# Kernel optimization log

Measured on AMD Instinct MI355X. Metric: run time of the kernel, lower is better.

The kernel has to match this reference:

```python
import jax, jax.numpy as jnp
import numpy as np

D_MODEL = 1024
NUM_HEADS = 16
D_K = D_MODEL // NUM_HEADS
D_FF = 4096
EPS = 1e-6


def setup_inputs() -> dict:
    key = jax.random.key(0)
    ks = jax.random.split(key, 12)
    B, S = 4, 1024
    s = 1.0 / np.sqrt(D_MODEL)
    return {
        "x": jax.random.normal(ks[0], (B, S, D_MODEL), dtype=jnp.float32),
        "ln1_g": jnp.ones((D_MODEL,), jnp.float32),
        "ln1_b": jnp.zeros((D_MODEL,), jnp.float32),
        "wq": jax.random.normal(ks[1], (D_MODEL, D_MODEL), jnp.float32) * s,
        "wk": jax.random.normal(ks[2], (D_MODEL, D_MODEL), jnp.float32) * s,
        "wv": jax.random.normal(ks[3], (D_MODEL, D_MODEL), jnp.float32) * s,
        "wo": jax.random.normal(ks[4], (D_MODEL, D_MODEL), jnp.float32) * s,
        "ln2_g": jnp.ones((D_MODEL,), jnp.float32),
        "ln2_b": jnp.zeros((D_MODEL,), jnp.float32),
        "w1": jax.random.normal(ks[5], (D_MODEL, D_FF), jnp.float32) * s,
        "b1": jnp.zeros((D_FF,), jnp.float32),
        "w2": jax.random.normal(ks[6], (D_FF, D_MODEL), jnp.float32) * (1.0 / np.sqrt(D_FF)),
        "b2": jnp.zeros((D_MODEL,), jnp.float32),
    }


def _layernorm(x, g, b):
    mu = jnp.mean(x, axis=-1, keepdims=True)
    var = jnp.var(x, axis=-1, keepdims=True)
    return (x - mu) * jax.lax.rsqrt(var + EPS) * g + b


def _mha(x, wq, wk, wv, wo):
    B, S, _ = x.shape
    # project and split heads: [B,S,D] -> [B,H,S,Dk]
    q = (x @ wq).reshape(B, S, NUM_HEADS, D_K).transpose(0, 2, 1, 3)
    k = (x @ wk).reshape(B, S, NUM_HEADS, D_K).transpose(0, 2, 1, 3)
    v = (x @ wv).reshape(B, S, NUM_HEADS, D_K).transpose(0, 2, 1, 3)
    scores = jnp.einsum("bhqd,bhkd->bhqk", q, k) / np.sqrt(D_K).astype(np.float32)
    attn = jax.nn.softmax(scores, axis=-1)  # no mask: source forwards mask=None
    out = jnp.einsum("bhqk,bhkd->bhqd", attn, v)
    out = out.transpose(0, 2, 1, 3).reshape(B, S, D_MODEL)
    return out @ wo


def reference(x, ln1_g, ln1_b, wq, wk, wv, wo, ln2_g, ln2_b, w1, b1, w2, b2):
    x1 = _layernorm(x, ln1_g, ln1_b)
    x = x + _mha(x1, wq, wk, wv, wo)  # dropout identity (eval)
    x2 = _layernorm(x, ln2_g, ln2_b)
    ffn = jax.nn.relu(x2 @ w1 + b1) @ w2 + b2
    return x + ffn
```

## Files before the change

### kernel.cpp

```cpp
#include <hip/hip_runtime.h>

typedef __bf16 bf16;
typedef __bf16 bf16x8 __attribute__((ext_vector_type(8)));
typedef __bf16 bf16x4 __attribute__((ext_vector_type(4)));
typedef float f32x4 __attribute__((ext_vector_type(4)));

__device__ __forceinline__ void gload_lds16(const void* g, void* l) {
  __builtin_amdgcn_global_load_lds(
      (const __attribute__((address_space(1))) unsigned int*)g,
      (__attribute__((address_space(3))) unsigned int*)l, 16, 0, 0);
}

__global__ __launch_bounds__(256) void prep_kernel(
    const float* __restrict__ wq, const float* __restrict__ wk,
    const float* __restrict__ wv, const float* __restrict__ wo,
    const float* __restrict__ w1, const float* __restrict__ w2,
    bf16* __restrict__ wTqkv, bf16* __restrict__ wTo,
    bf16* __restrict__ wT1, bf16* __restrict__ wT2,
    const float* __restrict__ x, const float* __restrict__ g,
    const float* __restrict__ b, bf16* __restrict__ y) {
  const int id = blockIdx.x;
  if (id < 1024) {
    const int w = threadIdx.x >> 6, lane = threadIdx.x & 63;
    const int row = id * 4 + w;
    const float* xr = x + (size_t)row * 1024;
    float4 v[4];
    float s = 0.f, sq = 0.f;
#pragma unroll
    for (int c = 0; c < 4; c++) {
      v[c] = *reinterpret_cast<const float4*>(xr + c * 256 + lane * 4);
      s += v[c].x + v[c].y + v[c].z + v[c].w;
      sq += v[c].x * v[c].x + v[c].y * v[c].y + v[c].z * v[c].z + v[c].w * v[c].w;
    }
#pragma unroll
    for (int d = 32; d >= 1; d >>= 1) {
      s += __shfl_xor(s, d, 64);
      sq += __shfl_xor(sq, d, 64);
    }
    const float mu = s * (1.f / 1024.f);
    const float rs = rsqrtf(sq * (1.f / 1024.f) - mu * mu + 1e-6f);
#pragma unroll
    for (int c = 0; c < 4; c++) {
      float4 gv = *reinterpret_cast<const float4*>(g + c * 256 + lane * 4);
      float4 bv = *reinterpret_cast<const float4*>(b + c * 256 + lane * 4);
      bf16x4 ov;
      ov[0] = (bf16)((v[c].x - mu) * rs * gv.x + bv.x);
      ov[1] = (bf16)((v[c].y - mu) * rs * gv.y + bv.y);
      ov[2] = (bf16)((v[c].z - mu) * rs * gv.z + bv.z);
      ov[3] = (bf16)((v[c].w - mu) * rs * gv.w + bv.w);
      *reinterpret_cast<bf16x4*>(y + (size_t)row * 1024 + c * 256 + lane * 4) = ov;
    }
    return;
  }
  __shared__ float tile[32][33];
  const int idx = id - 1024;
  const float* src;
  bf16* dst;
  int R, C, bx, by;
  if (idx < 4096) {
    const int m = idx >> 10, r = idx & 1023;
    src = m == 0 ? wq : m == 1 ? wk : m == 2 ? wv : wo;
    dst = m == 3 ? wTo : wTqkv + (size_t)m * 1024 * 1024;
    R = 1024; C = 1024; bx = r & 31; by = r >> 5;
  } else if (idx < 8192) {
    const int r = idx - 4096;
    src = w1; dst = wT1; R = 1024; C = 4096;
    bx = r & 127; by = r >> 7;
  } else {
    const int r = idx - 8192;
    src = w2; dst = wT2; R = 4096; C = 1024;
    bx = r & 31; by = r >> 5;
  }
  const int tx = threadIdx.x & 31, ty = threadIdx.x >> 5;
  const int c0 = bx * 32, r0 = by * 32;
#pragma unroll
  for (int i = 0; i < 4; i++)
    tile[ty + i * 8][tx] = src[(size_t)(r0 + ty + i * 8) * C + c0 + tx];
  __syncthreads();
#pragma unroll
  for (int i = 0; i < 4; i++)
    dst[(size_t)(c0 + ty + i * 8) * R + r0 + tx] = (bf16)tile[tx][ty + i * 8];
}

__global__ __launch_bounds__(256) void reduce_ln_kernel(const bf16* __restrict__ p0,
                                                        const bf16* __restrict__ p1,
                                                        const float* __restrict__ x,
                                                        const float* __restrict__ g,
                                                        const float* __restrict__ b,
                                                        float* __restrict__ xres,
                                                        bf16* __restrict__ y) {
  const int w = threadIdx.x >> 6, lane = threadIdx.x & 63;
  const int row = blockIdx.x * 4 + w;
  const size_t rb = (size_t)row * 1024;
  float4 v[4];
  float s = 0.f, sq = 0.f;
#pragma unroll
  for (int c = 0; c < 4; c++) {
    const int off = c * 256 + lane * 4;
    float4 xv = *reinterpret_cast<const float4*>(x + rb + off);
    bf16x4 a0 = *reinterpret_cast<const bf16x4*>(p0 + rb + off);
    bf16x4 a1 = *reinterpret_cast<const bf16x4*>(p1 + rb + off);
    v[c].x = xv.x + (float)a0[0] + (float)a1[0];
    v[c].y = xv.y + (float)a0[1] + (float)a1[1];
    v[c].z = xv.z + (float)a0[2] + (float)a1[2];
    v[c].w = xv.w + (float)a0[3] + (float)a1[3];
    *reinterpret_cast<float4*>(xres + rb + off) = v[c];
    s += v[c].x + v[c].y + v[c].z + v[c].w;
    sq += v[c].x * v[c].x + v[c].y * v[c].y + v[c].z * v[c].z + v[c].w * v[c].w;
  }
#pragma unroll
  for (int d = 32; d >= 1; d >>= 1) {
    s += __shfl_xor(s, d, 64);
    sq += __shfl_xor(sq, d, 64);
  }
  const float mu = s * (1.f / 1024.f);
  const float rs = rsqrtf(sq * (1.f / 1024.f) - mu * mu + 1e-6f);
#pragma unroll
  for (int c = 0; c < 4; c++) {
    const int off = c * 256 + lane * 4;
    float4 gv = *reinterpret_cast<const float4*>(g + off);
    float4 bv = *reinterpret_cast<const float4*>(b + off);
    bf16x4 ov;
    ov[0] = (bf16)((v[c].x - mu) * rs * gv.x + bv.x);
    ov[1] = (bf16)((v[c].y - mu) * rs * gv.y + bv.y);
    ov[2] = (bf16)((v[c].z - mu) * rs * gv.z + bv.z);
    ov[3] = (bf16)((v[c].w - mu) * rs * gv.w + bv.w);
    *reinterpret_cast<bf16x4*>(y + rb + off) = ov;
  }
}

__global__ __launch_bounds__(256) void reduce_out_kernel(const bf16* __restrict__ p0,
                                                         const bf16* __restrict__ p1,
                                                         const bf16* __restrict__ p2,
                                                         const bf16* __restrict__ p3,
                                                         const float* __restrict__ bias,
                                                         const float* __restrict__ xres,
                                                         float* __restrict__ out) {
  const size_t i = ((size_t)blockIdx.x * 256 + threadIdx.x) * 8;
  const int col = (int)(i & 1023);
  bf16x8 a0 = *reinterpret_cast<const bf16x8*>(p0 + i);
  bf16x8 a1 = *reinterpret_cast<const bf16x8*>(p1 + i);
  bf16x8 a2 = *reinterpret_cast<const bf16x8*>(p2 + i);
  bf16x8 a3 = *reinterpret_cast<const bf16x8*>(p3 + i);
  float4 r0 = *reinterpret_cast<const float4*>(xres + i);
  float4 r1 = *reinterpret_cast<const float4*>(xres + i + 4);
  float4 b0 = *reinterpret_cast<const float4*>(bias + col);
  float4 b1 = *reinterpret_cast<const float4*>(bias + col + 4);
  float4 o0, o1;
  o0.x = r0.x + b0.x + (float)a0[0] + (float)a1[0] + (float)a2[0] + (float)a3[0];
  o0.y = r0.y + b0.y + (float)a0[1] + (float)a1[1] + (float)a2[1] + (float)a3[1];
  o0.z = r0.z + b0.z + (float)a0[2] + (float)a1[2] + (float)a2[2] + (float)a3[2];
  o0.w = r0.w + b0.w + (float)a0[3] + (float)a1[3] + (float)a2[3] + (float)a3[3];
  o1.x = r1.x + b1.x + (float)a0[4] + (float)a1[4] + (float)a2[4] + (float)a3[4];
  o1.y = r1.y + b1.y + (float)a0[5] + (float)a1[5] + (float)a2[5] + (float)a3[5];
  o1.z = r1.z + b1.z + (float)a0[6] + (float)a1[6] + (float)a2[6] + (float)a3[6];
  o1.w = r1.w + b1.w + (float)a0[7] + (float)a1[7] + (float)a2[7] + (float)a3[7];
  *reinterpret_cast<float4*>(out + i) = o0;
  *reinterpret_cast<float4*>(out + i + 4) = o1;
}

template <int EPI>
__global__ __launch_bounds__(256) void gemm_bt(const bf16* __restrict__ A,
                                               const bf16* __restrict__ Bt,
                                               void* __restrict__ Cout,
                                               const float* __restrict__ bias,
                                               int M, int N, int K, int gy, int gxy,
                                               int Kc) {
  __shared__ __align__(16) bf16 As[2][128][32];
  __shared__ __align__(16) bf16 Bs[2][128][32];
  const int tid = threadIdx.x;
  const int w = tid >> 6, lane = tid & 63;
  const int wr = w >> 1, wc = w & 1;

  const int nwg = gridDim.x;
  const int cpx = nwg >> 3;
  const int swz = (blockIdx.x & 7) * cpx + (blockIdx.x >> 3);
  const int chunk = swz / gxy, rem = swz % gxy;
  const int gpc = gy << 3;
  const int band = rem / gpc, r2 = rem % gpc;
  const int bm = (band * 8 + (r2 & 7)) * 128;
  const int bn = (r2 >> 3) * 128;

  f32x4 acc[4][4] = {};
  const int r4 = lane >> 2;
  const int c8 = (lane & 3) * 8;
  const bf16* Ag = A + (size_t)(bm + w * 32 + r4) * K + chunk * Kc + c8;
  const bf16* Bg = Bt + (size_t)(bn + w * 32 + r4) * K + chunk * Kc + c8;
  const int fr = lane & 15, fo = (lane >> 4) * 8;

#define STAGE(buf, k0)                                                 \
  do {                                                                 \
    gload_lds16(Ag + (k0), &As[buf][w * 32][0]);                       \
    gload_lds16(Ag + (size_t)16 * K + (k0), &As[buf][w * 32 + 16][0]); \
    gload_lds16(Bg + (k0), &Bs[buf][w * 32][0]);                       \
    gload_lds16(Bg + (size_t)16 * K + (k0), &Bs[buf][w * 32 + 16][0]); \
  } while (0)

  const int nt = Kc >> 5;
  STAGE(0, 0);
  __syncthreads();
  int cur = 0;
  for (int t = 0; t < nt; ++t) {
    if (t + 1 < nt) STAGE(cur ^ 1, (t + 1) << 5);
    bf16x8 af[4], bfr[4];
#pragma unroll
    for (int m = 0; m < 4; m++)
      af[m] = *reinterpret_cast<const bf16x8*>(&As[cur][wr * 64 + m * 16 + fr][fo]);
#pragma unroll
    for (int n = 0; n < 4; n++)
      bfr[n] = *reinterpret_cast<const bf16x8*>(&Bs[cur][wc * 64 + n * 16 + fr][fo]);
#pragma unroll
    for (int m = 0; m < 4; m++)
#pragma unroll
      for (int n = 0; n < 4; n++)
        acc[m][n] = __builtin_amdgcn_mfma_f32_16x16x32_bf16(af[m], bfr[n], acc[m][n], 0, 0, 0);
    __syncthreads();
    cur ^= 1;
  }
#undef STAGE

  bf16* outp = (bf16*)Cout + (EPI == 3 ? (size_t)chunk * M * N : 0);
  const int cr = (lane >> 4) * 4, cc = lane & 15;
#pragma unroll
  for (int m = 0; m < 4; m++) {
#pragma unroll
    for (int n = 0; n < 4; n++) {
      const int row = bm + wr * 64 + m * 16 + cr;
      const int col = bn + wc * 64 + n * 16 + cc;
#pragma unroll
      for (int r = 0; r < 4; r++) {
        const float va = acc[m][n][r];
        const size_t idx = (size_t)(row + r) * N + col;
        if (EPI == 0 || EPI == 3) {
          outp[idx] = (bf16)va;
        } else {
          const float t = va + bias[col];
          outp[idx] = (bf16)(t > 0.f ? t : 0.f);
        }
      }
    }
  }
}

template <int EPI>
__global__ __launch_bounds__(512, 2) void gemm256(const bf16* __restrict__ A,
                                                  const bf16* __restrict__ Bt,
                                                  void* __restrict__ Cout,
                                                  const float* __restrict__ bias,
                                                  int M, int N, int K, int gy, int gxy,
                                                  int Kc) {
  __shared__ __align__(16) bf16 As[2][256][64];
  __shared__ __align__(16) bf16 Bs[2][256][64];
  const int tid = threadIdx.x;
  const int w = tid >> 6, lane = tid & 63;
  const int wm = w >> 2, wn = w & 3;
  const int fr = lane & 15, g = lane >> 4;

  const int nwg = gridDim.x;
  const int cpx = nwg >> 3;
  const int swz = (blockIdx.x & 7) * cpx + (blockIdx.x >> 3);
  const int chunk = swz / gxy, rem = swz % gxy;
  const int gpc = gy << 3;
  const int band = rem / gpc, r2 = rem % gpc;
  const int bm = (band * 8 + (r2 & 7)) * 256;
  const int bn = (r2 >> 3) * 256;

  const bf16* Ab = A + (size_t)bm * K;
  const bf16* Bb = Bt + (size_t)bn * K;

  const int lr = lane >> 3;
  const int sle = ((lane & 7) ^ lr) * 8;
  const int rB0 = w * 16;
  const int rB1 = 128 + w * 16;
  const int rA0 = wm * 128 + wn * 16;
  const int rA1 = wm * 128 + 64 + wn * 16;

  char* AsB = (char*)&As[0][0][0];
  char* BsB = (char*)&Bs[0][0][0];
  const int rowA = (wm * 128 + fr) * 128;
  const int rowB = (wn * 64 + fr) * 128;
  const int colk0 = (g * 16) ^ ((fr & 7) << 4);
  const int colk1 = (64 + g * 16) ^ ((fr & 7) << 4);

  f32x4 acc[8][4] = {};

#define SG8(base, r0, kb, ldsrow)                                           \
  do {                                                                      \
    gload_lds16(base + (size_t)((r0) + lr) * K + (kb) + sle, (ldsrow));     \
    gload_lds16(base + (size_t)((r0) + 8 + lr) * K + (kb) + sle,            \
                (char*)(ldsrow) + 1024);                                    \
  } while (0)

  const int nt = Kc >> 6;
  const int koff = chunk * Kc;

  SG8(Bb, rB0, koff, BsB + rB0 * 128);
  SG8(Bb, rB1, koff, BsB + rB1 * 128);
  SG8(Ab, rA0, koff, AsB + rA0 * 128);
  SG8(Ab, rA1, koff, AsB + rA1 * 128);

#define PHASE_BODY(p, mb)                                                     \
  {                                                                           \
    if ((p) == 0) {                                                           \
      _Pragma("unroll") for (int nf = 0; nf < 4; nf++) {                      \
        bfr[nf][0] = *(const bf16x8*)(Br + rowB + nf * 2048 + colk0);         \
        bfr[nf][1] = *(const bf16x8*)(Br + rowB + nf * 2048 + colk1);         \
      }                                                                       \
    }                                                                         \
    af[0][0] = *(const bf16x8*)(Ar + rowA + (mb)*2048 + colk0);               \
    af[0][1] = *(const bf16x8*)(Ar + rowA + (mb)*2048 + colk1);               \
    af[1][0] = *(const bf16x8*)(Ar + rowA + ((mb) + 1) * 2048 + colk0);       \
    af[1][1] = *(const bf16x8*)(Ar + rowA + ((mb) + 1) * 2048 + colk1);       \
    if (pre) {                                                                \
      if ((p) == 0) SG8(Bb, rB0, kb2, Bw + rB0 * 128);                        \
      if ((p) == 1) SG8(Bb, rB1, kb2, Bw + rB1 * 128);                        \
      if ((p) == 2) SG8(Ab, rA0, kb2, Aw + rA0 * 128);                        \
      if ((p) == 3) SG8(Ab, rA1, kb2, Aw + rA1 * 128);                        \
    }                                                                         \
    __builtin_amdgcn_s_setprio(1);                                            \
    _Pragma("unroll") for (int m2 = 0; m2 < 2; m2++)                          \
        _Pragma("unroll") for (int nf = 0; nf < 4; nf++) {                    \
      acc[(mb) + m2][nf] = __builtin_amdgcn_mfma_f32_16x16x32_bf16(           \
          af[m2][0], bfr[nf][0], acc[(mb) + m2][nf], 0, 0, 0);                \
      acc[(mb) + m2][nf] = __builtin_amdgcn_mfma_f32_16x16x32_bf16(           \
          af[m2][1], bfr[nf][1], acc[(mb) + m2][nf], 0, 0, 0);                \
    }                                                                         \
    __builtin_amdgcn_s_setprio(0);                                            \
  }

  int buf = 0;
  for (int kt = 0; kt < nt; ++kt) {
    char* Ar = AsB + buf * 32768;
    char* Br = BsB + buf * 32768;
    char* Aw = AsB + (buf ^ 1) * 32768;
    char* Bw = BsB + (buf ^ 1) * 32768;
    const bool pre = (kt + 1) < nt;
    const int kb2 = koff + (kt + 1) * 64;
    bf16x8 bfr[4][2];
    bf16x8 af[2][2];

    asm volatile("s_waitcnt vmcnt(2)" ::: "memory");
    __builtin_amdgcn_s_barrier();
    PHASE_BODY(0, 0)

    if (pre) asm volatile("s_waitcnt vmcnt(4)" ::: "memory");
    else     asm volatile("s_waitcnt vmcnt(2)" ::: "memory");
    __builtin_amdgcn_s_barrier();
    PHASE_BODY(1, 2)

    if (pre) asm volatile("s_waitcnt vmcnt(4)" ::: "memory");
    else     asm volatile("s_waitcnt vmcnt(0)" ::: "memory");
    __builtin_amdgcn_s_barrier();
    PHASE_BODY(2, 4)

    if (pre) asm volatile("s_waitcnt vmcnt(6)" ::: "memory");
    else     asm volatile("s_waitcnt vmcnt(0)" ::: "memory");
    __builtin_amdgcn_s_barrier();
    PHASE_BODY(3, 6)

    buf ^= 1;
  }
#undef PHASE_BODY
#undef SG8

  bf16* outp = (bf16*)Cout + (EPI == 3 ? (size_t)chunk * M * N : 0);
  const int cr = g * 4;
#pragma unroll
  for (int mf = 0; mf < 8; mf++) {
#pragma unroll
    for (int nf = 0; nf < 4; nf++) {
      const int row = bm + wm * 128 + mf * 16 + cr;
      const int col = bn + wn * 64 + nf * 16 + fr;
#pragma unroll
      for (int r = 0; r < 4; r++) {
        const float va = acc[mf][nf][r];
        const size_t idx = (size_t)(row + r) * N + col;
        if (EPI == 3 || EPI == 0) {
          outp[idx] = (bf16)va;
        } else {
          const float t = va + bias[col];
          outp[idx] = (bf16)(t > 0.f ? t : 0.f);
        }
      }
    }
  }
}

__global__ __launch_bounds__(512, 4) void attn_kernel(const bf16* __restrict__ Q,
                                                      const bf16* __restrict__ K,
                                                      const bf16* __restrict__ V,
                                                      bf16* __restrict__ O, int ld) {
  __shared__ __align__(16) bf16 Ks[2][64][64];
  __shared__ __align__(16) bf16 Vt[2][64][64];
  __shared__ __align__(16) bf16 Pl[8][16][64];
  const int tid = threadIdx.x;
  const int w = tid >> 6, l = tid & 63;
  const int lo = l & 15, g = l >> 4;
  const int sw = (lo & 7) << 3;

  const int id = blockIdx.x;
  const int bh = id & 63, qb = id >> 6;
  const int b = bh >> 4, h = bh & 15;
  const int hoff = h * 64;
  const size_t rowQ = (size_t)b * 1024 + qb * 128 + w * 16;
  const size_t rowKV0 = (size_t)b * 1024;

  const int srow = tid >> 3, scch = tid & 7;
  const int vcb = w * 8;

  bf16x8 qfr[2];
#pragma unroll
  for (int ds = 0; ds < 2; ds++)
    qfr[ds] = *reinterpret_cast<const bf16x8*>(
        Q + (rowQ + lo) * ld + hoff + ds * 32 + g * 8);

  const float c = 0.18033688f;
  f32x4 lacc = {0.f, 0.f, 0.f, 0.f};
  f32x4 o[4] = {};

  {
    gload_lds16(K + (rowKV0 + srow) * ld + hoff + ((scch ^ (srow & 7)) << 3),
                &Ks[0][w * 8][0]);
    bf16x8 vv = *reinterpret_cast<const bf16x8*>(V + (rowKV0 + l) * ld + hoff + vcb);
#pragma unroll
    for (int j = 0; j < 8; j++) Vt[0][vcb + j][l ^ (j << 3)] = vv[j];
  }
  __syncthreads();

#define ATILE(PAR, KT)                                                               \
  {                                                                                  \
    bf16x8 vv;                                                                       \
    const bool more = (KT) + 1 < 16;                                                 \
    if (more) {                                                                      \
      const size_t rkv = rowKV0 + ((KT) + 1) * 64;                                   \
      gload_lds16(K + (rkv + srow) * ld + hoff + ((scch ^ (srow & 7)) << 3),         \
                  &Ks[(PAR) ^ 1][w * 8][0]);                                         \
      vv = *reinterpret_cast<const bf16x8*>(V + (rkv + l) * ld + hoff + vcb);        \
    }                                                                                \
    f32x4 sa[4] = {};                                                                \
    _Pragma("unroll") for (int ds = 0; ds < 2; ds++) {                               \
      bf16x8 kf[4];                                                                  \
      _Pragma("unroll") for (int kfi = 0; kfi < 4; kfi++)                            \
          kf[kfi] = *reinterpret_cast<const bf16x8*>(                                \
              &Ks[PAR][kfi * 16 + lo][(ds * 32 + g * 8) ^ sw]);                      \
      _Pragma("unroll") for (int kfi = 0; kfi < 4; kfi++)                            \
          sa[kfi] =                                                                  \
              __builtin_amdgcn_mfma_f32_16x16x32_bf16(kf[kfi], qfr[ds], sa[kfi], 0, 0, 0); \
    }                                                                                \
    float p[16];                                                                     \
    _Pragma("unroll") for (int kfi = 0; kfi < 4; kfi++)                              \
        _Pragma("unroll") for (int r = 0; r < 4; r++)                                \
            p[kfi * 4 + r] = exp2f(sa[kfi][r] * c);                                  \
    _Pragma("unroll") for (int r = 0; r < 4; r++)                                    \
        lacc[r] += (p[r] + p[4 + r]) + (p[8 + r] + p[12 + r]);                       \
    _Pragma("unroll") for (int kfi = 0; kfi < 4; kfi++) {                            \
      bf16x4 pk;                                                                     \
      pk[0] = (bf16)p[kfi * 4 + 0];                                                  \
      pk[1] = (bf16)p[kfi * 4 + 1];                                                  \
      pk[2] = (bf16)p[kfi * 4 + 2];                                                  \
      pk[3] = (bf16)p[kfi * 4 + 3];                                                  \
      *reinterpret_cast<bf16x4*>(&Pl[w][lo][(kfi * 16 + g * 4) ^ sw]) = pk;          \
    }                                                                                \
    _Pragma("unroll") for (int ks = 0; ks < 2; ks++) {                               \
      bf16x8 pf = *reinterpret_cast<const bf16x8*>(&Pl[w][lo][(ks * 32 + g * 8) ^ sw]); \
      _Pragma("unroll") for (int df = 0; df < 4; df++) {                             \
        bf16x8 vf = *reinterpret_cast<const bf16x8*>(                                \
            &Vt[PAR][df * 16 + lo][(ks * 32 + g * 8) ^ sw]);                         \
        o[df] = __builtin_amdgcn_mfma_f32_16x16x32_bf16(vf, pf, o[df], 0, 0, 0);     \
      }                                                                              \
    }                                                                                \
    if (more) {                                                                      \
      _Pragma("unroll") for (int j = 0; j < 8; j++)                                  \
          Vt[(PAR) ^ 1][vcb + j][l ^ (j << 3)] = vv[j];                              \
    }                                                                                \
    __syncthreads();                                                                 \
  }

  for (int kt2 = 0; kt2 < 16; kt2 += 2) {
    ATILE(0, kt2)
    ATILE(1, kt2 + 1)
  }
#undef ATILE

  float lsum = (lacc[0] + lacc[1]) + (lacc[2] + lacc[3]);
  lsum += __shfl_xor(lsum, 16);
  lsum += __shfl_xor(lsum, 32);
  const float rl = 1.f / lsum;
#pragma unroll
  for (int df = 0; df < 4; df++) {
    bf16x4 ov;
#pragma unroll
    for (int r = 0; r < 4; r++) ov[r] = (bf16)(o[df][r] * rl);
    *reinterpret_cast<bf16x4*>(&Pl[w][lo][(df * 16 + g * 4) ^ sw]) = ov;
  }
  const int row = l >> 2;
  const int swr = (row & 7) << 3;
  const int c2 = (l & 3) * 16;
#pragma unroll
  for (int i = 0; i < 2; i++) {
    bf16x8 ov = *reinterpret_cast<const bf16x8*>(&Pl[w][row][(c2 + i * 8) ^ swr]);
    *reinterpret_cast<bf16x8*>(O + (rowQ + row) * 1024 + hoff + c2 + i * 8) = ov;
  }
}

extern "C" void kernel_launch(void* const* d_in, const int* in_sizes, int n_in,
                              void* d_out, int out_size, void* d_ws, size_t ws_size,
                              hipStream_t stream) {
  const float* x     = (const float*)d_in[0];
  const float* ln1_g = (const float*)d_in[1];
  const float* ln1_b = (const float*)d_in[2];
  const float* wq    = (const float*)d_in[3];
  const float* wk    = (const float*)d_in[4];
  const float* wv    = (const float*)d_in[5];
  const float* wo    = (const float*)d_in[6];
  const float* ln2_g = (const float*)d_in[7];
  const float* ln2_b = (const float*)d_in[8];
  const float* w1    = (const float*)d_in[9];
  const float* b1    = (const float*)d_in[10];
  const float* w2    = (const float*)d_in[11];
  const float* b2    = (const float*)d_in[12];

  const size_t MB = 1ull << 20;
  char* ws = (char*)d_ws;
  bf16* wTqkv = (bf16*)(ws + 0 * MB);
  bf16* wTo   = (bf16*)(ws + 6 * MB);
  bf16* wT1   = (bf16*)(ws + 8 * MB);
  bf16* wT2   = (bf16*)(ws + 16 * MB);
  bf16* x1    = (bf16*)(ws + 24 * MB);
  bf16* qkv   = (bf16*)(ws + 32 * MB);
  float* xres = (float*)(ws + 56 * MB);
  bf16* h1    = (bf16*)(ws + 72 * MB);
  bf16* attn  = x1;
  bf16* x2    = qkv;
  bf16* pOp   = (bf16*)(ws + 40 * MB);
  bf16* pF    = (bf16*)(ws + 24 * MB);

  const dim3 TB(256);

  prep_kernel<<<13312, TB, 0, stream>>>(wq, wk, wv, wo, w1, w2,
                                        wTqkv, wTo, wT1, wT2,
                                        x, ln1_g, ln1_b, x1);

  gemm256<0><<<192, dim3(512), 0, stream>>>(x1, wTqkv, qkv, nullptr, 4096, 3072, 1024, 12, 192, 1024);

  attn_kernel<<<512, dim3(512), 0, stream>>>(qkv, qkv + 1024, qkv + 2048, attn, 3072);

  gemm_bt<3><<<512, TB, 0, stream>>>(attn, wTo, pOp, nullptr, 4096, 1024, 1024, 8, 256, 512);

  reduce_ln_kernel<<<1024, TB, 0, stream>>>(pOp, pOp + 4096 * 1024, x, ln2_g, ln2_b, xres, x2);

  gemm256<2><<<256, dim3(512), 0, stream>>>(x2, wT1, h1, b1, 4096, 4096, 1024, 16, 256, 1024);

  gemm256<3><<<256, dim3(512), 0, stream>>>(h1, wT2, pF, nullptr, 4096, 1024, 4096, 4, 64, 1024);

  reduce_out_kernel<<<2048, TB, 0, stream>>>(pF, pF + 4096 * 1024, pF + 2 * 4096 * 1024,
                                             pF + 3 * 4096 * 1024, b2, xres, (float*)d_out);
}
```

Before: 196.7 us.

## Overlap FFN weight transposes with QKV GEMM and store residual in bf16

Moves the w1/w2 transpose-to-bf16 work out of the prep kernel into extra workgroups of the QKV GEMM launch, using CUs left idle by its 192 tiles. Also stores the post-attention residual as bf16 instead of fp32 to cut memory traffic in the two reduce kernels. The aux blocks do many serial transposes and could lengthen the GEMM launch. The bf16 residual lowers output precision.

```diff
diff --git a/kernel.cpp b/kernel.cpp
--- a/kernel.cpp
+++ b/kernel.cpp
@@ -14,9 +14,7 @@
 __global__ __launch_bounds__(256) void prep_kernel(
     const float* __restrict__ wq, const float* __restrict__ wk,
     const float* __restrict__ wv, const float* __restrict__ wo,
-    const float* __restrict__ w1, const float* __restrict__ w2,
     bf16* __restrict__ wTqkv, bf16* __restrict__ wTo,
-    bf16* __restrict__ wT1, bf16* __restrict__ wT2,
     const float* __restrict__ x, const float* __restrict__ g,
     const float* __restrict__ b, bf16* __restrict__ y) {
   const int id = blockIdx.x;
@@ -54,32 +52,18 @@
   }
   __shared__ float tile[32][33];
   const int idx = id - 1024;
-  const float* src;
-  bf16* dst;
-  int R, C, bx, by;
-  if (idx < 4096) {
-    const int m = idx >> 10, r = idx & 1023;
-    src = m == 0 ? wq : m == 1 ? wk : m == 2 ? wv : wo;
-    dst = m == 3 ? wTo : wTqkv + (size_t)m * 1024 * 1024;
-    R = 1024; C = 1024; bx = r & 31; by = r >> 5;
-  } else if (idx < 8192) {
-    const int r = idx - 4096;
-    src = w1; dst = wT1; R = 1024; C = 4096;
-    bx = r & 127; by = r >> 7;
-  } else {
-    const int r = idx - 8192;
-    src = w2; dst = wT2; R = 4096; C = 1024;
-    bx = r & 31; by = r >> 5;
-  }
+  const int m = idx >> 10, r = idx & 1023;
+  const float* src = m == 0 ? wq : m == 1 ? wk : m == 2 ? wv : wo;
+  bf16* dst = m == 3 ? wTo : wTqkv + (size_t)m * 1024 * 1024;
   const int tx = threadIdx.x & 31, ty = threadIdx.x >> 5;
-  const int c0 = bx * 32, r0 = by * 32;
+  const int c0 = (r & 31) * 32, r0 = (r >> 5) * 32;
 #pragma unroll
   for (int i = 0; i < 4; i++)
-    tile[ty + i * 8][tx] = src[(size_t)(r0 + ty + i * 8) * C + c0 + tx];
+    tile[ty + i * 8][tx] = src[(size_t)(r0 + ty + i * 8) * 1024 + c0 + tx];
   __syncthreads();
 #pragma unroll
   for (int i = 0; i < 4; i++)
-    dst[(size_t)(c0 + ty + i * 8) * R + r0 + tx] = (bf16)tile[tx][ty + i * 8];
+    dst[(size_t)(c0 + ty + i * 8) * 1024 + r0 + tx] = (bf16)tile[tx][ty + i * 8];
 }
 
 __global__ __launch_bounds__(256) void reduce_ln_kernel(const bf16* __restrict__ p0,
@@ -87,7 +71,7 @@
                                                         const float* __restrict__ x,
                                                         const float* __restrict__ g,
                                                         const float* __restrict__ b,
-                                                        float* __restrict__ xres,
+                                                        bf16* __restrict__ xres,
                                                         bf16* __restrict__ y) {
   const int w = threadIdx.x >> 6, lane = threadIdx.x & 63;
   const int row = blockIdx.x * 4 + w;
@@ -104,7 +88,10 @@
     v[c].y = xv.y + (float)a0[1] + (float)a1[1];
     v[c].z = xv.z + (float)a0[2] + (float)a1[2];
     v[c].w = xv.w + (float)a0[3] + (float)a1[3];
-    *reinterpret_cast<float4*>(xres + rb + off) = v[c];
+    bf16x4 xo;
+    xo[0] = (bf16)v[c].x; xo[1] = (bf16)v[c].y;
+    xo[2] = (bf16)v[c].z; xo[3] = (bf16)v[c].w;
+    *reinterpret_cast<bf16x4*>(xres + rb + off) = xo;
     s += v[c].x + v[c].y + v[c].z + v[c].w;
     sq += v[c].x * v[c].x + v[c].y * v[c].y + v[c].z * v[c].z + v[c].w * v[c].w;
   }
@@ -134,7 +121,7 @@
                                                          const bf16* __restrict__ p2,
                                                          const bf16* __restrict__ p3,
                                                          const float* __restrict__ bias,
-                                                         const float* __restrict__ xres,
+                                                         const bf16* __restrict__ xres,
                                                          float* __restrict__ out) {
   const size_t i = ((size_t)blockIdx.x * 256 + threadIdx.x) * 8;
   const int col = (int)(i & 1023);
@@ -142,19 +129,18 @@
   bf16x8 a1 = *reinterpret_cast<const bf16x8*>(p1 + i);
   bf16x8 a2 = *reinterpret_cast<const bf16x8*>(p2 + i);
   bf16x8 a3 = *reinterpret_cast<const bf16x8*>(p3 + i);
-  float4 r0 = *reinterpret_cast<const float4*>(xres + i);
-  float4 r1 = *reinterpret_cast<const float4*>(xres + i + 4);
+  bf16x8 xr = *reinterpret_cast<const bf16x8*>(xres + i);
   float4 b0 = *reinterpret_cast<const float4*>(bias + col);
   float4 b1 = *reinterpret_cast<const float4*>(bias + col + 4);
   float4 o0, o1;
-  o0.x = r0.x + b0.x + (float)a0[0] + (float)a1[0] + (float)a2[0] + (float)a3[0];
-  o0.y = r0.y + b0.y + (float)a0[1] + (float)a1[1] + (float)a2[1] + (float)a3[1];
-  o0.z = r0.z + b0.z + (float)a0[2] + (float)a1[2] + (float)a2[2] + (float)a3[2];
-  o0.w = r0.w + b0.w + (float)a0[3] + (float)a1[3] + (float)a2[3] + (float)a3[3];
-  o1.x = r1.x + b1.x + (float)a0[4] + (float)a1[4] + (float)a2[4] + (float)a3[4];
-  o1.y = r1.y + b1.y + (float)a0[5] + (float)a1[5] + (float)a2[5] + (float)a3[5];
-  o1.z = r1.z + b1.z + (float)a0[6] + (float)a1[6] + (float)a2[6] + (float)a3[6];
-  o1.w = r1.w + b1.w + (float)a0[7] + (float)a1[7] + (float)a2[7] + (float)a3[7];
+  o0.x = (float)xr[0] + b0.x + (float)a0[0] + (float)a1[0] + (float)a2[0] + (float)a3[0];
+  o0.y = (float)xr[1] + b0.y + (float)a0[1] + (float)a1[1] + (float)a2[1] + (float)a3[1];
+  o0.z = (float)xr[2] + b0.z + (float)a0[2] + (float)a1[2] + (float)a2[2] + (float)a3[2];
+  o0.w = (float)xr[3] + b0.w + (float)a0[3] + (float)a1[3] + (float)a2[3] + (float)a3[3];
+  o1.x = (float)xr[4] + b1.x + (float)a0[4] + (float)a1[4] + (float)a2[4] + (float)a3[4];
+  o1.y = (float)xr[5] + b1.y + (float)a0[5] + (float)a1[5] + (float)a2[5] + (float)a3[5];
+  o1.z = (float)xr[6] + b1.z + (float)a0[6] + (float)a1[6] + (float)a2[6] + (float)a3[6];
+  o1.w = (float)xr[7] + b1.w + (float)a0[7] + (float)a1[7] + (float)a2[7] + (float)a3[7];
   *reinterpret_cast<float4*>(out + i) = o0;
   *reinterpret_cast<float4*>(out + i + 4) = o1;
 }
@@ -248,7 +234,11 @@
                                                   void* __restrict__ Cout,
                                                   const float* __restrict__ bias,
                                                   int M, int N, int K, int gy, int gxy,
-                                                  int Kc) {
+                                                  int Kc, int ngemm,
+                                                  const float* __restrict__ tw1,
+                                                  const float* __restrict__ tw2,
+                                                  bf16* __restrict__ two1,
+                                                  bf16* __restrict__ two2) {
   __shared__ __align__(16) bf16 As[2][256][64];
   __shared__ __align__(16) bf16 Bs[2][256][64];
   const int tid = threadIdx.x;
@@ -259,6 +249,41 @@
   const int nwg = gridDim.x;
   const int cpx = nwg >> 3;
   const int swz = (blockIdx.x & 7) * cpx + (blockIdx.x >> 3);
+
+  char* AsB = (char*)&As[0][0][0];
+  char* BsB = (char*)&Bs[0][0][0];
+
+  if (swz >= ngemm) {
+    const int aux = swz - ngemm;
+    float* tf = (float*)AsB + (tid >> 8) * (32 * 33);
+    const int t8 = tid & 255;
+    const int tx = t8 & 31, ty = t8 >> 5;
+    for (int t = 0; t < 64; ++t) {
+      const int job = t * 128 + aux * 2 + (tid >> 8);
+      const float* src;
+      bf16* dst;
+      int R, C, bx, by;
+      if (job < 4096) {
+        src = tw1; dst = two1; R = 1024; C = 4096;
+        bx = job & 127; by = job >> 7;
+      } else {
+        const int j2 = job - 4096;
+        src = tw2; dst = two2; R = 4096; C = 1024;
+        bx = j2 & 31; by = j2 >> 5;
+      }
+      const int c0 = bx * 32, r0 = by * 32;
+#pragma unroll
+      for (int i = 0; i < 4; i++)
+        tf[(ty + i * 8) * 33 + tx] = src[(size_t)(r0 + ty + i * 8) * C + c0 + tx];
+      __syncthreads();
+#pragma unroll
+      for (int i = 0; i < 4; i++)
+        dst[(size_t)(c0 + ty + i * 8) * R + r0 + tx] = (bf16)tf[tx * 33 + ty + i * 8];
+      __syncthreads();
+    }
+    return;
+  }
+
   const int chunk = swz / gxy, rem = swz % gxy;
   const int gpc = gy << 3;
   const int band = rem / gpc, r2 = rem % gpc;
@@ -275,8 +300,6 @@
   const int rA0 = wm * 128 + wn * 16;
   const int rA1 = wm * 128 + 64 + wn * 16;
 
-  char* AsB = (char*)&As[0][0][0];
-  char* BsB = (char*)&Bs[0][0][0];
   const int rowA = (wm * 128 + fr) * 128;
   const int rowB = (wn * 64 + fr) * 128;
   const int colk0 = (g * 16) ^ ((fr & 7) << 4);
@@ -528,7 +551,7 @@
   bf16* wT2   = (bf16*)(ws + 16 * MB);
   bf16* x1    = (bf16*)(ws + 24 * MB);
   bf16* qkv   = (bf16*)(ws + 32 * MB);
-  float* xres = (float*)(ws + 56 * MB);
+  bf16* xres  = (bf16*)(ws + 56 * MB);
   bf16* h1    = (bf16*)(ws + 72 * MB);
   bf16* attn  = x1;
   bf16* x2    = qkv;
@@ -537,11 +560,12 @@
 
   const dim3 TB(256);
 
-  prep_kernel<<<13312, TB, 0, stream>>>(wq, wk, wv, wo, w1, w2,
-                                        wTqkv, wTo, wT1, wT2,
-                                        x, ln1_g, ln1_b, x1);
-
-  gemm256<0><<<192, dim3(512), 0, stream>>>(x1, wTqkv, qkv, nullptr, 4096, 3072, 1024, 12, 192, 1024);
+  prep_kernel<<<5120, TB, 0, stream>>>(wq, wk, wv, wo, wTqkv, wTo,
+                                       x, ln1_g, ln1_b, x1);
+
+  gemm256<0><<<256, dim3(512), 0, stream>>>(x1, wTqkv, qkv, nullptr,
+                                            4096, 3072, 1024, 12, 192, 1024, 192,
+                                            w1, w2, wT1, wT2);
 
   attn_kernel<<<512, dim3(512), 0, stream>>>(qkv, qkv + 1024, qkv + 2048, attn, 3072);
 
@@ -549,9 +573,13 @@
 
   reduce_ln_kernel<<<1024, TB, 0, stream>>>(pOp, pOp + 4096 * 1024, x, ln2_g, ln2_b, xres, x2);
 
-  gemm256<2><<<256, dim3(512), 0, stream>>>(x2, wT1, h1, b1, 4096, 4096, 1024, 16, 256, 1024);
-
-  gemm256<3><<<256, dim3(512), 0, stream>>>(h1, wT2, pF, nullptr, 4096, 1024, 4096, 4, 64, 1024);
+  gemm256<2><<<256, dim3(512), 0, stream>>>(x2, wT1, h1, b1,
+                                            4096, 4096, 1024, 16, 256, 1024, 256,
+                                            nullptr, nullptr, nullptr, nullptr);
+
+  gemm256<3><<<256, dim3(512), 0, stream>>>(h1, wT2, pF, nullptr,
+                                            4096, 1024, 4096, 4, 64, 1024, 256,
+                                            nullptr, nullptr, nullptr, nullptr);
 
   reduce_out_kernel<<<2048, TB, 0, stream>>>(pF, pF + 4096 * 1024, pF + 2 * 4096 * 1024,
                                              pF + 3 * 4096 * 1024, b2, xres, (float*)d_out);
```

Measured after the change: 200.3 us. About the same (+1.8%).
